# Kernel tuning notes

Measured on AMD Instinct MI355X. Metric: run time of the kernel, lower is better.

## Reference

```python
import jax, jax.numpy as jnp
import numpy as np

N = 8192
IN_F = 256
OUT_F = 128


def setup_inputs() -> dict:
    key = jax.random.key(0)
    k1, k2, k3, k4, k5, k6 = jax.random.split(key, 6)
    input = jax.random.normal(k1, (N, IN_F), dtype=jnp.float32)
    adj = jax.random.randint(k2, (N, N), 0, 2, dtype=jnp.int32)
    # xavier-uniform-like init scaled by gain=0.5
    def xavier(k, shape, gain=0.5):
        fan_in, fan_out = shape[0], shape[1]
        lim = gain * np.sqrt(6.0 / (fan_in + fan_out))
        return jax.random.uniform(k, shape, dtype=jnp.float32, minval=-lim, maxval=lim)
    W_s = xavier(k3, (IN_F, OUT_F))
    a_s = xavier(k4, (OUT_F, 1))
    W_n = xavier(k5, (IN_F, OUT_F))
    a_n = xavier(k6, (OUT_F, 1))
    return {"input": input, "adj": adj, "W_s": W_s, "a_s": a_s, "W_n": W_n, "a_n": a_n}


def reference(input, adj, W_s, a_s, W_n, a_n):
    # Projections: [N, out_features]
    h_s = input @ W_s
    h_n = input @ W_n
    # Additive attention logits: e[i, j] = relu((h_s @ a_s)[i] + (h_n @ a_n)[j])
    e = jax.nn.relu((h_s @ a_s) + (h_n @ a_n).T)  # [N, N]
    # Masked softmax over neighbors (dim=1)
    attention = jnp.where(adj > 0, e, jnp.float32(-9e15))
    attention = jax.nn.softmax(attention, axis=1)
    # Self-scaling term (sum of softmax rows, kept for faithfulness)
    attention_sum = jnp.sum(attention, axis=-1, keepdims=True)
    attention_s = 1.0 / (1.0 + attention_sum)
    # Dropout is identity in eval mode (p=0 / training=False)
    h_prime = attention_s * h_s + attention @ h_n
    # concat=True -> elu activation
    return jax.nn.elu(h_prime)
```

## Files before the change

### kernel.cpp

```cpp
#include <hip/hip_runtime.h>
#include <math.h>

#define NN 8192

typedef short short8 __attribute__((ext_vector_type(8)));
typedef float f32x4 __attribute__((ext_vector_type(4)));

__device__ __forceinline__ float eluf(float x) {
  return x > 0.f ? x : (__expf(x) - 1.f);
}
__device__ __forceinline__ unsigned short f2bf(float f) {
  union { float f; unsigned u; } v; v.f = f;
  unsigned r = v.u + 0x7fffu + ((v.u >> 16) & 1u);
  return (unsigned short)(r >> 16);
}

__global__ __launch_bounds__(256) void k_pack(const int* __restrict__ A,
                                              unsigned* __restrict__ P) {
  const int t = threadIdx.x;
  const int row = blockIdx.x;
  const int4* src = (const int4*)(A + (size_t)row * NN) + t * 8;
  int4 v[8];
#pragma unroll
  for (int c = 0; c < 8; ++c) v[c] = src[c];
  unsigned w = 0;
#pragma unroll
  for (int c = 0; c < 8; ++c) {
    w |= (unsigned)(v[c].x & 1) << (c * 4 + 0);
    w |= (unsigned)(v[c].y & 1) << (c * 4 + 1);
    w |= (unsigned)(v[c].z & 1) << (c * 4 + 2);
    w |= (unsigned)(v[c].w & 1) << (c * 4 + 3);
  }
  P[(size_t)row * 256 + t] = w;
}

__global__ __launch_bounds__(256) void k_proj(const float* __restrict__ X,
                                              const float* __restrict__ Ws,
                                              const float* __restrict__ Wn,
                                              const float* __restrict__ as_,
                                              const float* __restrict__ an_,
                                              float* __restrict__ Hs,
                                              unsigned short* __restrict__ HnT,
                                              float* __restrict__ s_out,
                                              float* __restrict__ n_out) {
  __shared__ float4 lin4[8 * 64];
  const int t = threadIdx.x;
  const int i0 = blockIdx.x * 8;
  const float4* Xg = (const float4*)X + (size_t)i0 * 64;
  lin4[t] = Xg[t];
  if (t < 256) lin4[t + 256] = Xg[t + 256];
  __syncthreads();
  const int c = t & 127;
  const int rh = t >> 7;
  float accs[4], accn[4];
#pragma unroll
  for (int r = 0; r < 4; ++r) { accs[r] = 0.f; accn[r] = 0.f; }
  for (int k = 0; k < 256; k += 4) {
    float ws0 = Ws[(k + 0) * 128 + c], ws1 = Ws[(k + 1) * 128 + c];
    float ws2 = Ws[(k + 2) * 128 + c], ws3 = Ws[(k + 3) * 128 + c];
    float wn0 = Wn[(k + 0) * 128 + c], wn1 = Wn[(k + 1) * 128 + c];
    float wn2 = Wn[(k + 2) * 128 + c], wn3 = Wn[(k + 3) * 128 + c];
#pragma unroll
    for (int r = 0; r < 4; ++r) {
      float4 iv = lin4[(rh * 4 + r) * 64 + (k >> 2)];
      accs[r] = fmaf(iv.x, ws0, accs[r]); accs[r] = fmaf(iv.y, ws1, accs[r]);
      accs[r] = fmaf(iv.z, ws2, accs[r]); accs[r] = fmaf(iv.w, ws3, accs[r]);
      accn[r] = fmaf(iv.x, wn0, accn[r]); accn[r] = fmaf(iv.y, wn1, accn[r]);
      accn[r] = fmaf(iv.z, wn2, accn[r]); accn[r] = fmaf(iv.w, wn3, accn[r]);
    }
  }
#pragma unroll
  for (int r = 0; r < 4; ++r)
    Hs[(size_t)(i0 + rh * 4 + r) * 128 + c] = accs[r];
  {
    union { unsigned short us[4]; ushort4 u4; } pk;
#pragma unroll
    for (int r = 0; r < 4; ++r) pk.us[r] = f2bf(accn[r]);
    *(ushort4*)(HnT + (size_t)blockIdx.x * 1024 + c * 8 + rh * 4) = pk.u4;
  }
  float* red = (float*)lin4;
  const int wv = t >> 6, ln = t & 63;
  __syncthreads();
  {
    float av = as_[c];
#pragma unroll
    for (int r = 0; r < 4; ++r) red[(rh * 4 + r) * 128 + c] = accs[r] * av;
  }
  __syncthreads();
#pragma unroll
  for (int h = 0; h < 2; ++h) {
    int row = wv * 2 + h;
    float p = red[row * 128 + ln] + red[row * 128 + 64 + ln];
#pragma unroll
    for (int off = 32; off >= 1; off >>= 1) p += __shfl_down(p, off);
    if (ln == 0) s_out[i0 + row] = p;
  }
  __syncthreads();
  {
    float av = an_[c];
#pragma unroll
    for (int r = 0; r < 4; ++r) red[(rh * 4 + r) * 128 + c] = accn[r] * av;
  }
  __syncthreads();
#pragma unroll
  for (int h = 0; h < 2; ++h) {
    int row = wv * 2 + h;
    float p = red[row * 128 + ln] + red[row * 128 + 64 + ln];
#pragma unroll
    for (int off = 32; off >= 1; off >>= 1) p += __shfl_down(p, off);
    if (ln == 0) n_out[i0 + row] = p;
  }
}

__global__ __launch_bounds__(512, 4) void k_main_bits(const unsigned* __restrict__ Pk,
                                                      const unsigned short* __restrict__ HnT,
                                                      const float* __restrict__ sv_g,
                                                      const float* __restrict__ nv_g,
                                                      float* __restrict__ HsOut) {
  __shared__ float accbuf[8][16][128];
  __shared__ float zsh[8][16];
  __shared__ float zf[16];

  const int t = threadIdx.x;
  const int wv = t >> 6;
  const int ln = t & 63;
  const int q = ln >> 4;
  const int m = ln & 15;
  const int row0 = blockIdx.x * 16;

  const float sm = sv_g[row0 + m];
  const int jbase = wv * 1024 + q * 8;
  const float* nptr = nv_g + jbase;
  const unsigned* Pp = Pk + (size_t)(row0 + m) * 256 + wv * 32;
  const unsigned short* bptr = HnT + ((size_t)(wv * 128 + q) * 128 + m) * 8;

  f32x4 acc[8];
#pragma unroll
  for (int ft = 0; ft < 8; ++ft) acc[ft] = (f32x4){0.f, 0.f, 0.f, 0.f};
  float zp = 0.f;

  float4 nvv[2][2];
  unsigned bv[2];
  union Breg { uint4 u; short8 s; };
  Breg breg[8];

  nvv[0][0] = *(const float4*)(nptr);      nvv[0][1] = *(const float4*)(nptr + 4);
  nvv[1][0] = *(const float4*)(nptr + 32); nvv[1][1] = *(const float4*)(nptr + 36);
  bv[0] = Pp[0];
  bv[1] = Pp[1];
  breg[0].u = *(const uint4*)(bptr);       breg[1].u = *(const uint4*)(bptr + 128);
  breg[2].u = *(const uint4*)(bptr + 256); breg[3].u = *(const uint4*)(bptr + 384);
  breg[4].u = *(const uint4*)(bptr + 512); breg[5].u = *(const uint4*)(bptr + 640);
  breg[6].u = *(const uint4*)(bptr + 768); breg[7].u = *(const uint4*)(bptr + 896);

#pragma unroll 2
  for (int tt = 0; tt < 32; ++tt) {
    const int cur = tt & 1;
    short8 fr;
    {
      float nvl[8] = {nvv[cur][0].x, nvv[cur][0].y, nvv[cur][0].z, nvv[cur][0].w,
                      nvv[cur][1].x, nvv[cur][1].y, nvv[cur][1].z, nvv[cur][1].w};
      const unsigned byte = (bv[cur] >> (q * 8)) & 0xffu;
#pragma unroll
      for (int k = 0; k < 8; ++k) {
        float w = ((byte >> k) & 1u) ? __expf(fmaxf(sm + nvl[k], 0.f)) : 0.f;
        zp += w;
        fr[k] = (short)f2bf(w);
      }
    }
    if (tt < 30) {
      const float* p = nptr + (tt + 2) * 32;
      nvv[cur][0] = *(const float4*)p;
      nvv[cur][1] = *(const float4*)(p + 4);
      bv[cur] = Pp[tt + 2];
    }
    __builtin_amdgcn_s_setprio(1);
    acc[0] = __builtin_amdgcn_mfma_f32_16x16x32_bf16(fr, breg[0].s, acc[0], 0, 0, 0);
    acc[1] = __builtin_amdgcn_mfma_f32_16x16x32_bf16(fr, breg[1].s, acc[1], 0, 0, 0);
    acc[2] = __builtin_amdgcn_mfma_f32_16x16x32_bf16(fr, breg[2].s, acc[2], 0, 0, 0);
    acc[3] = __builtin_amdgcn_mfma_f32_16x16x32_bf16(fr, breg[3].s, acc[3], 0, 0, 0);
    acc[4] = __builtin_amdgcn_mfma_f32_16x16x32_bf16(fr, breg[4].s, acc[4], 0, 0, 0);
    acc[5] = __builtin_amdgcn_mfma_f32_16x16x32_bf16(fr, breg[5].s, acc[5], 0, 0, 0);
    acc[6] = __builtin_amdgcn_mfma_f32_16x16x32_bf16(fr, breg[6].s, acc[6], 0, 0, 0);
    acc[7] = __builtin_amdgcn_mfma_f32_16x16x32_bf16(fr, breg[7].s, acc[7], 0, 0, 0);
    __builtin_amdgcn_s_setprio(0);
    if (tt < 31) {
      const unsigned short* p = bptr + (size_t)(tt + 1) * 4096;
      breg[0].u = *(const uint4*)(p);       breg[1].u = *(const uint4*)(p + 128);
      breg[2].u = *(const uint4*)(p + 256); breg[3].u = *(const uint4*)(p + 384);
      breg[4].u = *(const uint4*)(p + 512); breg[5].u = *(const uint4*)(p + 640);
      breg[6].u = *(const uint4*)(p + 768); breg[7].u = *(const uint4*)(p + 896);
    }
  }

  {
    float zz = zp;
    zz += __shfl_down(zz, 32);
    zz += __shfl_down(zz, 16);
    if (ln < 16) zsh[wv][ln] = zz;
  }
#pragma unroll
  for (int ft = 0; ft < 8; ++ft) {
#pragma unroll
    for (int reg = 0; reg < 4; ++reg)
      accbuf[wv][q * 4 + reg][ft * 16 + m] = acc[ft][reg];
  }
  __syncthreads();
  if (t < 16) {
    float z = zsh[0][t] + zsh[1][t] + zsh[2][t] + zsh[3][t] +
              zsh[4][t] + zsh[5][t] + zsh[6][t] + zsh[7][t];
    zf[t] = 1.f / z;
  }
  __syncthreads();
  {
    const int row = t >> 5;
    const int f0 = (t & 31) * 4;
    f32x4 ssum = *(const f32x4*)&accbuf[0][row][f0];
#pragma unroll
    for (int w = 1; w < 8; ++w) ssum += *(const f32x4*)&accbuf[w][row][f0];
    const float invz = zf[row];
    const size_t off = (size_t)(row0 + row) * 128 + f0;
    float4 h = *(const float4*)(HsOut + off);
    float4 o;
    o.x = eluf(fmaf(ssum[0], invz, 0.5f * h.x));
    o.y = eluf(fmaf(ssum[1], invz, 0.5f * h.y));
    o.z = eluf(fmaf(ssum[2], invz, 0.5f * h.z));
    o.w = eluf(fmaf(ssum[3], invz, 0.5f * h.w));
    *(float4*)(HsOut + off) = o;
  }
}

__global__ __launch_bounds__(512, 4) void k_main_adj(const int* __restrict__ A,
                                                     const unsigned short* __restrict__ HnT,
                                                     const float* __restrict__ sv_g,
                                                     const float* __restrict__ nv_g,
                                                     float* __restrict__ HsOut) {
  __shared__ float accbuf[8][16][128];
  __shared__ float zsh[8][16];
  __shared__ float zf[16];

  const int t = threadIdx.x;
  const int wv = t >> 6;
  const int ln = t & 63;
  const int q = ln >> 4;
  const int m = ln & 15;
  const int row0 = blockIdx.x * 16;

  const float sm = sv_g[row0 + m];
  const int jbase = wv * 1024 + q * 8;
  const int* aptr = A + (size_t)(row0 + m) * NN + jbase;
  const float* nptr = nv_g + jbase;
  const unsigned short* bptr = HnT + ((size_t)(wv * 128 + q) * 128 + m) * 8;

  f32x4 acc[8];
#pragma unroll
  for (int ft = 0; ft < 8; ++ft) acc[ft] = (f32x4){0.f, 0.f, 0.f, 0.f};
  float zp = 0.f;

  int4 adjv[2][2];
  float4 nvv[2][2];
  union Breg { uint4 u; short8 s; };
  Breg breg[8];

  adjv[0][0] = *(const int4*)(aptr);       adjv[0][1] = *(const int4*)(aptr + 4);
  adjv[1][0] = *(const int4*)(aptr + 32);  adjv[1][1] = *(const int4*)(aptr + 36);
  nvv[0][0] = *(const float4*)(nptr);      nvv[0][1] = *(const float4*)(nptr + 4);
  breg[0].u = *(const uint4*)(bptr);       breg[1].u = *(const uint4*)(bptr + 128);
  breg[2].u = *(const uint4*)(bptr + 256); breg[3].u = *(const uint4*)(bptr + 384);
  breg[4].u = *(const uint4*)(bptr + 512); breg[5].u = *(const uint4*)(bptr + 640);
  breg[6].u = *(const uint4*)(bptr + 768); breg[7].u = *(const uint4*)(bptr + 896);

#pragma unroll 2
  for (int tt = 0; tt < 32; ++tt) {
    const int cur = tt & 1;
    short8 fr;
    {
      float nvl[8] = {nvv[cur][0].x, nvv[cur][0].y, nvv[cur][0].z, nvv[cur][0].w,
                      nvv[cur][1].x, nvv[cur][1].y, nvv[cur][1].z, nvv[cur][1].w};
      int av[8] = {adjv[cur][0].x, adjv[cur][0].y, adjv[cur][0].z, adjv[cur][0].w,
                   adjv[cur][1].x, adjv[cur][1].y, adjv[cur][1].z, adjv[cur][1].w};
#pragma unroll
      for (int k = 0; k < 8; ++k) {
        float w = av[k] > 0 ? __expf(fmaxf(sm + nvl[k], 0.f)) : 0.f;
        zp += w;
        fr[k] = (short)f2bf(w);
      }
    }
    if (tt < 31) {
      const float* p = nptr + (tt + 1) * 32;
      nvv[cur ^ 1][0] = *(const float4*)p;
      nvv[cur ^ 1][1] = *(const float4*)(p + 4);
    }
    __builtin_amdgcn_s_setprio(1);
    acc[0] = __builtin_amdgcn_mfma_f32_16x16x32_bf16(fr, breg[0].s, acc[0], 0, 0, 0);
    acc[1] = __builtin_amdgcn_mfma_f32_16x16x32_bf16(fr, breg[1].s, acc[1], 0, 0, 0);
    acc[2] = __builtin_amdgcn_mfma_f32_16x16x32_bf16(fr, breg[2].s, acc[2], 0, 0, 0);
    acc[3] = __builtin_amdgcn_mfma_f32_16x16x32_bf16(fr, breg[3].s, acc[3], 0, 0, 0);
    acc[4] = __builtin_amdgcn_mfma_f32_16x16x32_bf16(fr, breg[4].s, acc[4], 0, 0, 0);
    acc[5] = __builtin_amdgcn_mfma_f32_16x16x32_bf16(fr, breg[5].s, acc[5], 0, 0, 0);
    acc[6] = __builtin_amdgcn_mfma_f32_16x16x32_bf16(fr, breg[6].s, acc[6], 0, 0, 0);
    acc[7] = __builtin_amdgcn_mfma_f32_16x16x32_bf16(fr, breg[7].s, acc[7], 0, 0, 0);
    __builtin_amdgcn_s_setprio(0);
    if (tt < 31) {
      const unsigned short* p = bptr + (size_t)(tt + 1) * 4096;
      breg[0].u = *(const uint4*)(p);       breg[1].u = *(const uint4*)(p + 128);
      breg[2].u = *(const uint4*)(p + 256); breg[3].u = *(const uint4*)(p + 384);
      breg[4].u = *(const uint4*)(p + 512); breg[5].u = *(const uint4*)(p + 640);
      breg[6].u = *(const uint4*)(p + 768); breg[7].u = *(const uint4*)(p + 896);
    }
    if (tt < 30) {
      const int* p = aptr + (tt + 2) * 32;
      adjv[cur][0] = *(const int4*)p;
      adjv[cur][1] = *(const int4*)(p + 4);
    }
  }

  {
    float zz = zp;
    zz += __shfl_down(zz, 32);
    zz += __shfl_down(zz, 16);
    if (ln < 16) zsh[wv][ln] = zz;
  }
#pragma unroll
  for (int ft = 0; ft < 8; ++ft) {
#pragma unroll
    for (int reg = 0; reg < 4; ++reg)
      accbuf[wv][q * 4 + reg][ft * 16 + m] = acc[ft][reg];
  }
  __syncthreads();
  if (t < 16) {
    float z = zsh[0][t] + zsh[1][t] + zsh[2][t] + zsh[3][t] +
              zsh[4][t] + zsh[5][t] + zsh[6][t] + zsh[7][t];
    zf[t] = 1.f / z;
  }
  __syncthreads();
  {
    const int row = t >> 5;
    const int f0 = (t & 31) * 4;
    f32x4 ssum = *(const f32x4*)&accbuf[0][row][f0];
#pragma unroll
    for (int w = 1; w < 8; ++w) ssum += *(const f32x4*)&accbuf[w][row][f0];
    const float invz = zf[row];
    const size_t off = (size_t)(row0 + row) * 128 + f0;
    float4 h = *(const float4*)(HsOut + off);
    float4 o;
    o.x = eluf(fmaf(ssum[0], invz, 0.5f * h.x));
    o.y = eluf(fmaf(ssum[1], invz, 0.5f * h.y));
    o.z = eluf(fmaf(ssum[2], invz, 0.5f * h.z));
    o.w = eluf(fmaf(ssum[3], invz, 0.5f * h.w));
    *(float4*)(HsOut + off) = o;
  }
}

extern "C" void kernel_launch(void* const* d_in, const int* in_sizes, int n_in,
                              void* d_out, int out_size, void* d_ws, size_t ws_size,
                              hipStream_t stream) {
  const float* X   = (const float*)d_in[0];
  const int*   A   = (const int*)d_in[1];
  const float* Ws  = (const float*)d_in[2];
  const float* as_ = (const float*)d_in[3];
  const float* Wn  = (const float*)d_in[4];
  const float* an_ = (const float*)d_in[5];
  float* out = (float*)d_out;

  unsigned short* HnT = (unsigned short*)d_ws;
  float* s = (float*)(HnT + (size_t)128 * NN);
  float* n = s + NN;
  unsigned* P = (unsigned*)(n + NN);

  const size_t base_need = (size_t)128 * NN * 2 + (size_t)2 * NN * 4;
  const size_t bits_need = base_need + (size_t)NN * 256 * 4;

  k_proj<<<1024, 256, 0, stream>>>(X, Ws, Wn, as_, an_, out, HnT, s, n);
  if (ws_size >= bits_need) {
    k_pack<<<8192, 256, 0, stream>>>(A, P);
    k_main_bits<<<512, 512, 0, stream>>>(P, HnT, s, n, out);
  } else {
    k_main_adj<<<512, 512, 0, stream>>>(A, HnT, s, n, out);
  }
}
```

Before: 451.9 us.

## Stage attention logits and adjacency bits in LDS; ballot-based coalesced bit packing

The pack kernel now reads the int adjacency matrix with fully coalesced per-lane loads and builds the bitmask words with wavefront ballots, replacing strided int4 loads. The bitmask main kernel preloads the whole neighbour-logit vector and the block's 16 rows of packed bits into a 64 KB LDS buffer, then reads them from LDS in the inner loop instead of from global memory. The accumulation buffer reuses the same LDS after a barrier, and the HnT register prefetch is split so loads are interleaved with the MFMA sequence. The larger LDS footprint may limit how many blocks fit per compute unit, and the upfront staging adds a latency bubble before compute starts.

```diff
diff --git a/kernel.cpp b/kernel.cpp
--- a/kernel.cpp
+++ b/kernel.cpp
@@ -17,21 +17,18 @@
 
 __global__ __launch_bounds__(256) void k_pack(const int* __restrict__ A,
                                               unsigned* __restrict__ P) {
-  const int t = threadIdx.x;
+  const int t = threadIdx.x, ln = t & 63, wv = t >> 6;
   const int row = blockIdx.x;
-  const int4* src = (const int4*)(A + (size_t)row * NN) + t * 8;
-  int4 v[8];
-#pragma unroll
-  for (int c = 0; c < 8; ++c) v[c] = src[c];
-  unsigned w = 0;
-#pragma unroll
-  for (int c = 0; c < 8; ++c) {
-    w |= (unsigned)(v[c].x & 1) << (c * 4 + 0);
-    w |= (unsigned)(v[c].y & 1) << (c * 4 + 1);
-    w |= (unsigned)(v[c].z & 1) << (c * 4 + 2);
-    w |= (unsigned)(v[c].w & 1) << (c * 4 + 3);
-  }
-  P[(size_t)row * 256 + t] = w;
+  const int* src = A + (size_t)row * NN + wv * 2048 + ln;
+  unsigned myw = 0;
+#pragma unroll
+  for (int c = 0; c < 32; ++c) {
+    int a = src[c * 64];
+    unsigned long long m = __ballot(a & 1);
+    if (ln == 2 * c)     myw = (unsigned)m;
+    if (ln == 2 * c + 1) myw = (unsigned)(m >> 32);
+  }
+  P[(size_t)row * 256 + wv * 64 + ln] = myw;
 }
 
 __global__ __launch_bounds__(256) void k_proj(const float* __restrict__ X,
@@ -117,7 +114,10 @@
                                                       const float* __restrict__ sv_g,
                                                       const float* __restrict__ nv_g,
                                                       float* __restrict__ HsOut) {
-  __shared__ float accbuf[8][16][128];
+  __shared__ __align__(16) char smem[65536];
+  float* nv_lds = (float*)smem;
+  unsigned* bits_lds = (unsigned*)(smem + 32768);
+  float* accbuf = (float*)smem;
   __shared__ float zsh[8][16];
   __shared__ float zf[16];
 
@@ -128,10 +128,158 @@
   const int m = ln & 15;
   const int row0 = blockIdx.x * 16;
 
+  {
+    float4* dst = (float4*)nv_lds;
+    const float4* s4 = (const float4*)nv_g;
+#pragma unroll
+    for (int k = 0; k < 4; ++k) dst[t + k * 512] = s4[t + k * 512];
+#pragma unroll
+    for (int k = 0; k < 8; ++k) {
+      int g = t + k * 512;
+      int rr = g >> 8;
+      int c8 = g & 255;
+      unsigned w = Pk[(size_t)(row0 + rr) * 256 + c8];
+      bits_lds[(c8 >> 5) * 512 + (c8 & 31) * 16 + rr] = w;
+    }
+  }
+
+  const float sm = sv_g[row0 + m];
+  const unsigned short* bp = HnT + ((size_t)(wv * 128 + q) * 128 + m) * 8;
+  const float* nvl = nv_lds + wv * 1024 + q * 8;
+  const unsigned* bts = bits_lds + wv * 512 + m;
+
+  f32x4 acc[8];
+#pragma unroll
+  for (int ft = 0; ft < 8; ++ft) acc[ft] = (f32x4){0.f, 0.f, 0.f, 0.f};
+  float zp = 0.f;
+
+  union Breg { uint4 u; short8 s; };
+  Breg breg[8];
+
+  __syncthreads();
+
+  breg[0].u = *(const uint4*)(bp);       breg[1].u = *(const uint4*)(bp + 128);
+  breg[2].u = *(const uint4*)(bp + 256); breg[3].u = *(const uint4*)(bp + 384);
+  breg[4].u = *(const uint4*)(bp + 512); breg[5].u = *(const uint4*)(bp + 640);
+  breg[6].u = *(const uint4*)(bp + 768); breg[7].u = *(const uint4*)(bp + 896);
+
+#pragma unroll 2
+  for (int tt = 0; tt < 31; ++tt) {
+    short8 fr;
+    {
+      float4 nv0 = *(const float4*)(nvl + tt * 32);
+      float4 nv1 = *(const float4*)(nvl + tt * 32 + 4);
+      const unsigned bw = bts[tt * 16];
+      const unsigned byte = (bw >> (q * 8)) & 0xffu;
+      float nvlv[8] = {nv0.x, nv0.y, nv0.z, nv0.w, nv1.x, nv1.y, nv1.z, nv1.w};
+#pragma unroll
+      for (int k = 0; k < 8; ++k) {
+        float w = ((byte >> k) & 1u) ? __expf(fmaxf(sm + nvlv[k], 0.f)) : 0.f;
+        zp += w;
+        fr[k] = (short)f2bf(w);
+      }
+    }
+    const unsigned short* np = bp + 4096;
+    __builtin_amdgcn_s_setprio(1);
+    acc[0] = __builtin_amdgcn_mfma_f32_16x16x32_bf16(fr, breg[0].s, acc[0], 0, 0, 0);
+    acc[1] = __builtin_amdgcn_mfma_f32_16x16x32_bf16(fr, breg[1].s, acc[1], 0, 0, 0);
+    acc[2] = __builtin_amdgcn_mfma_f32_16x16x32_bf16(fr, breg[2].s, acc[2], 0, 0, 0);
+    acc[3] = __builtin_amdgcn_mfma_f32_16x16x32_bf16(fr, breg[3].s, acc[3], 0, 0, 0);
+    breg[0].u = *(const uint4*)(np);       breg[1].u = *(const uint4*)(np + 128);
+    breg[2].u = *(const uint4*)(np + 256); breg[3].u = *(const uint4*)(np + 384);
+    acc[4] = __builtin_amdgcn_mfma_f32_16x16x32_bf16(fr, breg[4].s, acc[4], 0, 0, 0);
+    acc[5] = __builtin_amdgcn_mfma_f32_16x16x32_bf16(fr, breg[5].s, acc[5], 0, 0, 0);
+    acc[6] = __builtin_amdgcn_mfma_f32_16x16x32_bf16(fr, breg[6].s, acc[6], 0, 0, 0);
+    acc[7] = __builtin_amdgcn_mfma_f32_16x16x32_bf16(fr, breg[7].s, acc[7], 0, 0, 0);
+    __builtin_amdgcn_s_setprio(0);
+    breg[4].u = *(const uint4*)(np + 512); breg[5].u = *(const uint4*)(np + 640);
+    breg[6].u = *(const uint4*)(np + 768); breg[7].u = *(const uint4*)(np + 896);
+    bp = np;
+  }
+  {
+    short8 fr;
+    {
+      float4 nv0 = *(const float4*)(nvl + 31 * 32);
+      float4 nv1 = *(const float4*)(nvl + 31 * 32 + 4);
+      const unsigned bw = bts[31 * 16];
+      const unsigned byte = (bw >> (q * 8)) & 0xffu;
+      float nvlv[8] = {nv0.x, nv0.y, nv0.z, nv0.w, nv1.x, nv1.y, nv1.z, nv1.w};
+#pragma unroll
+      for (int k = 0; k < 8; ++k) {
+        float w = ((byte >> k) & 1u) ? __expf(fmaxf(sm + nvlv[k], 0.f)) : 0.f;
+        zp += w;
+        fr[k] = (short)f2bf(w);
+      }
+    }
+    __builtin_amdgcn_s_setprio(1);
+    acc[0] = __builtin_amdgcn_mfma_f32_16x16x32_bf16(fr, breg[0].s, acc[0], 0, 0, 0);
+    acc[1] = __builtin_amdgcn_mfma_f32_16x16x32_bf16(fr, breg[1].s, acc[1], 0, 0, 0);
+    acc[2] = __builtin_amdgcn_mfma_f32_16x16x32_bf16(fr, breg[2].s, acc[2], 0, 0, 0);
+    acc[3] = __builtin_amdgcn_mfma_f32_16x16x32_bf16(fr, breg[3].s, acc[3], 0, 0, 0);
+    acc[4] = __builtin_amdgcn_mfma_f32_16x16x32_bf16(fr, breg[4].s, acc[4], 0, 0, 0);
+    acc[5] = __builtin_amdgcn_mfma_f32_16x16x32_bf16(fr, breg[5].s, acc[5], 0, 0, 0);
+    acc[6] = __builtin_amdgcn_mfma_f32_16x16x32_bf16(fr, breg[6].s, acc[6], 0, 0, 0);
+    acc[7] = __builtin_amdgcn_mfma_f32_16x16x32_bf16(fr, breg[7].s, acc[7], 0, 0, 0);
+    __builtin_amdgcn_s_setprio(0);
+  }
+
+  {
+    float zz = zp;
+    zz += __shfl_down(zz, 32);
+    zz += __shfl_down(zz, 16);
+    if (ln < 16) zsh[wv][ln] = zz;
+  }
+  __syncthreads();
+#pragma unroll
+  for (int ft = 0; ft < 8; ++ft) {
+#pragma unroll
+    for (int reg = 0; reg < 4; ++reg)
+      accbuf[wv * 2048 + (q * 4 + reg) * 128 + ft * 16 + m] = acc[ft][reg];
+  }
+  if (t < 16) {
+    float z = zsh[0][t] + zsh[1][t] + zsh[2][t] + zsh[3][t] +
+              zsh[4][t] + zsh[5][t] + zsh[6][t] + zsh[7][t];
+    zf[t] = 1.f / z;
+  }
+  __syncthreads();
+  {
+    const int row = t >> 5;
+    const int f0 = (t & 31) * 4;
+    f32x4 ssum = *(const f32x4*)&accbuf[row * 128 + f0];
+#pragma unroll
+    for (int w = 1; w < 8; ++w) ssum += *(const f32x4*)&accbuf[w * 2048 + row * 128 + f0];
+    const float invz = zf[row];
+    const size_t off = (size_t)(row0 + row) * 128 + f0;
+    float4 h = *(const float4*)(HsOut + off);
+    float4 o;
+    o.x = eluf(fmaf(ssum[0], invz, 0.5f * h.x));
+    o.y = eluf(fmaf(ssum[1], invz, 0.5f * h.y));
+    o.z = eluf(fmaf(ssum[2], invz, 0.5f * h.z));
+    o.w = eluf(fmaf(ssum[3], invz, 0.5f * h.w));
+    *(float4*)(HsOut + off) = o;
+  }
+}
+
+__global__ __launch_bounds__(512, 4) void k_main_adj(const int* __restrict__ A,
+                                                     const unsigned short* __restrict__ HnT,
+                                                     const float* __restrict__ sv_g,
+                                                     const float* __restrict__ nv_g,
+                                                     float* __restrict__ HsOut) {
+  __shared__ float accbuf[8][16][128];
+  __shared__ float zsh[8][16];
+  __shared__ float zf[16];
+
+  const int t = threadIdx.x;
+  const int wv = t >> 6;
+  const int ln = t & 63;
+  const int q = ln >> 4;
+  const int m = ln & 15;
+  const int row0 = blockIdx.x * 16;
+
   const float sm = sv_g[row0 + m];
   const int jbase = wv * 1024 + q * 8;
+  const int* aptr = A + (size_t)(row0 + m) * NN + jbase;
   const float* nptr = nv_g + jbase;
-  const unsigned* Pp = Pk + (size_t)(row0 + m) * 256 + wv * 32;
   const unsigned short* bptr = HnT + ((size_t)(wv * 128 + q) * 128 + m) * 8;
 
   f32x4 acc[8];
@@ -139,15 +287,14 @@
   for (int ft = 0; ft < 8; ++ft) acc[ft] = (f32x4){0.f, 0.f, 0.f, 0.f};
   float zp = 0.f;
 
+  int4 adjv[2][2];
   float4 nvv[2][2];
-  unsigned bv[2];
   union Breg { uint4 u; short8 s; };
   Breg breg[8];
 
+  adjv[0][0] = *(const int4*)(aptr);       adjv[0][1] = *(const int4*)(aptr + 4);
+  adjv[1][0] = *(const int4*)(aptr + 32);  adjv[1][1] = *(const int4*)(aptr + 36);
   nvv[0][0] = *(const float4*)(nptr);      nvv[0][1] = *(const float4*)(nptr + 4);
-  nvv[1][0] = *(const float4*)(nptr + 32); nvv[1][1] = *(const float4*)(nptr + 36);
-  bv[0] = Pp[0];
-  bv[1] = Pp[1];
   breg[0].u = *(const uint4*)(bptr);       breg[1].u = *(const uint4*)(bptr + 128);
   breg[2].u = *(const uint4*)(bptr + 256); breg[3].u = *(const uint4*)(bptr + 384);
   breg[4].u = *(const uint4*)(bptr + 512); breg[5].u = *(const uint4*)(bptr + 640);
@@ -160,19 +307,19 @@
     {
       float nvl[8] = {nvv[cur][0].x, nvv[cur][0].y, nvv[cur][0].z, nvv[cur][0].w,
                       nvv[cur][1].x, nvv[cur][1].y, nvv[cur][1].z, nvv[cur][1].w};
-      const unsigned byte = (bv[cur] >> (q * 8)) & 0xffu;
+      int av[8] = {adjv[cur][0].x, adjv[cur][0].y, adjv[cur][0].z, adjv[cur][0].w,
+                   adjv[cur][1].x, adjv[cur][1].y, adjv[cur][1].z, adjv[cur][1].w};
 #pragma unroll
       for (int k = 0; k < 8; ++k) {
-        float w = ((byte >> k) & 1u) ? __expf(fmaxf(sm + nvl[k], 0.f)) : 0.f;
+        float w = av[k] > 0 ? __expf(fmaxf(sm + nvl[k], 0.f)) : 0.f;
         zp += w;
         fr[k] = (short)f2bf(w);
       }
     }
-    if (tt < 30) {
-      const float* p = nptr + (tt + 2) * 32;
-      nvv[cur][0] = *(const float4*)p;
-      nvv[cur][1] = *(const float4*)(p + 4);
-      bv[cur] = Pp[tt + 2];
+    if (tt < 31) {
+      const float* p = nptr + (tt + 1) * 32;
+      nvv[cur ^ 1][0] = *(const float4*)p;
+      nvv[cur ^ 1][1] = *(const float4*)(p + 4);
     }
     __builtin_amdgcn_s_setprio(1);
     acc[0] = __builtin_amdgcn_mfma_f32_16x16x32_bf16(fr, breg[0].s, acc[0], 0, 0, 0);
@@ -191,6 +338,11 @@
       breg[4].u = *(const uint4*)(p + 512); breg[5].u = *(const uint4*)(p + 640);
       breg[6].u = *(const uint4*)(p + 768); breg[7].u = *(const uint4*)(p + 896);
     }
+    if (tt < 30) {
+      const int* p = aptr + (tt + 2) * 32;
+      adjv[cur][0] = *(const int4*)p;
+      adjv[cur][1] = *(const int4*)(p + 4);
+    }
   }
 
   {
@@ -230,128 +382,6 @@
   }
 }
 
-__global__ __launch_bounds__(512, 4) void k_main_adj(const int* __restrict__ A,
-                                                     const unsigned short* __restrict__ HnT,
-                                                     const float* __restrict__ sv_g,
-                                                     const float* __restrict__ nv_g,
-                                                     float* __restrict__ HsOut) {
-  __shared__ float accbuf[8][16][128];
-  __shared__ float zsh[8][16];
-  __shared__ float zf[16];
-
-  const int t = threadIdx.x;
-  const int wv = t >> 6;
-  const int ln = t & 63;
-  const int q = ln >> 4;
-  const int m = ln & 15;
-  const int row0 = blockIdx.x * 16;
-
-  const float sm = sv_g[row0 + m];
-  const int jbase = wv * 1024 + q * 8;
-  const int* aptr = A + (size_t)(row0 + m) * NN + jbase;
-  const float* nptr = nv_g + jbase;
-  const unsigned short* bptr = HnT + ((size_t)(wv * 128 + q) * 128 + m) * 8;
-
-  f32x4 acc[8];
-#pragma unroll
-  for (int ft = 0; ft < 8; ++ft) acc[ft] = (f32x4){0.f, 0.f, 0.f, 0.f};
-  float zp = 0.f;
-
-  int4 adjv[2][2];
-  float4 nvv[2][2];
-  union Breg { uint4 u; short8 s; };
-  Breg breg[8];
-
-  adjv[0][0] = *(const int4*)(aptr);       adjv[0][1] = *(const int4*)(aptr + 4);
-  adjv[1][0] = *(const int4*)(aptr + 32);  adjv[1][1] = *(const int4*)(aptr + 36);
-  nvv[0][0] = *(const float4*)(nptr);      nvv[0][1] = *(const float4*)(nptr + 4);
-  breg[0].u = *(const uint4*)(bptr);       breg[1].u = *(const uint4*)(bptr + 128);
-  breg[2].u = *(const uint4*)(bptr + 256); breg[3].u = *(const uint4*)(bptr + 384);
-  breg[4].u = *(const uint4*)(bptr + 512); breg[5].u = *(const uint4*)(bptr + 640);
-  breg[6].u = *(const uint4*)(bptr + 768); breg[7].u = *(const uint4*)(bptr + 896);
-
-#pragma unroll 2
-  for (int tt = 0; tt < 32; ++tt) {
-    const int cur = tt & 1;
-    short8 fr;
-    {
-      float nvl[8] = {nvv[cur][0].x, nvv[cur][0].y, nvv[cur][0].z, nvv[cur][0].w,
-                      nvv[cur][1].x, nvv[cur][1].y, nvv[cur][1].z, nvv[cur][1].w};
-      int av[8] = {adjv[cur][0].x, adjv[cur][0].y, adjv[cur][0].z, adjv[cur][0].w,
-                   adjv[cur][1].x, adjv[cur][1].y, adjv[cur][1].z, adjv[cur][1].w};
-#pragma unroll
-      for (int k = 0; k < 8; ++k) {
-        float w = av[k] > 0 ? __expf(fmaxf(sm + nvl[k], 0.f)) : 0.f;
-        zp += w;
-        fr[k] = (short)f2bf(w);
-      }
-    }
-    if (tt < 31) {
-      const float* p = nptr + (tt + 1) * 32;
-      nvv[cur ^ 1][0] = *(const float4*)p;
-      nvv[cur ^ 1][1] = *(const float4*)(p + 4);
-    }
-    __builtin_amdgcn_s_setprio(1);
-    acc[0] = __builtin_amdgcn_mfma_f32_16x16x32_bf16(fr, breg[0].s, acc[0], 0, 0, 0);
-    acc[1] = __builtin_amdgcn_mfma_f32_16x16x32_bf16(fr, breg[1].s, acc[1], 0, 0, 0);
-    acc[2] = __builtin_amdgcn_mfma_f32_16x16x32_bf16(fr, breg[2].s, acc[2], 0, 0, 0);
-    acc[3] = __builtin_amdgcn_mfma_f32_16x16x32_bf16(fr, breg[3].s, acc[3], 0, 0, 0);
-    acc[4] = __builtin_amdgcn_mfma_f32_16x16x32_bf16(fr, breg[4].s, acc[4], 0, 0, 0);
-    acc[5] = __builtin_amdgcn_mfma_f32_16x16x32_bf16(fr, breg[5].s, acc[5], 0, 0, 0);
-    acc[6] = __builtin_amdgcn_mfma_f32_16x16x32_bf16(fr, breg[6].s, acc[6], 0, 0, 0);
-    acc[7] = __builtin_amdgcn_mfma_f32_16x16x32_bf16(fr, breg[7].s, acc[7], 0, 0, 0);
-    __builtin_amdgcn_s_setprio(0);
-    if (tt < 31) {
-      const unsigned short* p = bptr + (size_t)(tt + 1) * 4096;
-      breg[0].u = *(const uint4*)(p);       breg[1].u = *(const uint4*)(p + 128);
-      breg[2].u = *(const uint4*)(p + 256); breg[3].u = *(const uint4*)(p + 384);
-      breg[4].u = *(const uint4*)(p + 512); breg[5].u = *(const uint4*)(p + 640);
-      breg[6].u = *(const uint4*)(p + 768); breg[7].u = *(const uint4*)(p + 896);
-    }
-    if (tt < 30) {
-      const int* p = aptr + (tt + 2) * 32;
-      adjv[cur][0] = *(const int4*)p;
-      adjv[cur][1] = *(const int4*)(p + 4);
-    }
-  }
-
-  {
-    float zz = zp;
-    zz += __shfl_down(zz, 32);
-    zz += __shfl_down(zz, 16);
-    if (ln < 16) zsh[wv][ln] = zz;
-  }
-#pragma unroll
-  for (int ft = 0; ft < 8; ++ft) {
-#pragma unroll
-    for (int reg = 0; reg < 4; ++reg)
-      accbuf[wv][q * 4 + reg][ft * 16 + m] = acc[ft][reg];
-  }
-  __syncthreads();
-  if (t < 16) {
-    float z = zsh[0][t] + zsh[1][t] + zsh[2][t] + zsh[3][t] +
-              zsh[4][t] + zsh[5][t] + zsh[6][t] + zsh[7][t];
-    zf[t] = 1.f / z;
-  }
-  __syncthreads();
-  {
-    const int row = t >> 5;
-    const int f0 = (t & 31) * 4;
-    f32x4 ssum = *(const f32x4*)&accbuf[0][row][f0];
-#pragma unroll
-    for (int w = 1; w < 8; ++w) ssum += *(const f32x4*)&accbuf[w][row][f0];
-    const float invz = zf[row];
-    const size_t off = (size_t)(row0 + row) * 128 + f0;
-    float4 h = *(const float4*)(HsOut + off);
-    float4 o;
-    o.x = eluf(fmaf(ssum[0], invz, 0.5f * h.x));
-    o.y = eluf(fmaf(ssum[1], invz, 0.5f * h.y));
-    o.z = eluf(fmaf(ssum[2], invz, 0.5f * h.z));
-    o.w = eluf(fmaf(ssum[3], invz, 0.5f * h.w));
-    *(float4*)(HsOut + off) = o;
-  }
-}
-
 extern "C" void kernel_launch(void* const* d_in, const int* in_sizes, int n_in,
                               void* d_out, int out_size, void* d_ws, size_t ws_size,
                               hipStream_t stream) {
```

Result: slower. 618.0 us (+36.7%).
